# Kernel optimization log

Hardware: AMD Instinct MI355X
Metric: run time of the kernel (lower is better)

Reference implementation:

```python
import jax, jax.numpy as jnp
import numpy as np

NUM_CONCAT = 3

def setup_inputs() -> dict:
    key = jax.random.key(0)
    k1, k2, k3 = jax.random.split(key, 3)
    x = jax.random.normal(k1, (4, 2048, 4096), dtype=jnp.float32)
    W = jax.random.normal(k2, (12288, 4096), dtype=jnp.float32) * 0.02
    b = jax.random.normal(k3, (12288,), dtype=jnp.float32) * 0.02
    return {"x": x, "W": W, "b": b}

def reference(x, W, b):
    # Fused concat-linear: one GEMM over the concatenated weight, then split.
    # x: [B, S, D]; W: [NUM_CONCAT*H, D]; b: [NUM_CONCAT*H]
    y = jnp.einsum('bsd,od->bso', x, W) + b  # [B, S, NUM_CONCAT*H]
    hidden = y.shape[-1] // NUM_CONCAT
    return tuple(y[..., i * hidden:(i + 1) * hidden] for i in range(NUM_CONCAT))
```

## Files before the change

kernel.cpp:

```cpp
#include <hip/hip_runtime.h>
#include <stdint.h>


typedef __attribute__((ext_vector_type(8))) short short8;
typedef __attribute__((ext_vector_type(4))) float f32x4;

#define BM  256
#define BN  256
#define BKT 64

__device__ __forceinline__ unsigned short f2bf(float f) {
  union { float f; unsigned u; } v; v.f = f;
  unsigned u = v.u;
  u += 0x7FFFu + ((u >> 16) & 1u);
  return (unsigned short)(u >> 16);
}

__global__ __launch_bounds__(256)
void cast_all_f32_to_bf16(const float* __restrict__ a, unsigned long long na4,
                          unsigned short* __restrict__ oa,
                          const float* __restrict__ b, unsigned long long nb4,
                          unsigned short* __restrict__ ob) {
  const unsigned long long stride = (unsigned long long)gridDim.x * blockDim.x;
  const unsigned long long i0 = (unsigned long long)blockIdx.x * blockDim.x + threadIdx.x;
  for (unsigned long long k = i0; k < na4; k += stride) {
    float4 v = ((const float4*)a)[k];
    uint2 o;
    o.x = (unsigned)f2bf(v.x) | ((unsigned)f2bf(v.y) << 16);
    o.y = (unsigned)f2bf(v.z) | ((unsigned)f2bf(v.w) << 16);
    ((uint2*)oa)[k] = o;
  }
  for (unsigned long long k = i0; k < nb4; k += stride) {
    float4 v = ((const float4*)b)[k];
    uint2 o;
    o.x = (unsigned)f2bf(v.x) | ((unsigned)f2bf(v.y) << 16);
    o.y = (unsigned)f2bf(v.z) | ((unsigned)f2bf(v.w) << 16);
    ((uint2*)ob)[k] = o;
  }
}

__device__ __forceinline__ void gload16(const unsigned short* src, short* dst) {
  __builtin_amdgcn_global_load_lds(
      (const __attribute__((address_space(1))) unsigned int*)src,
      (__attribute__((address_space(3))) unsigned int*)dst, 16, 0, 0);
}

__global__ __launch_bounds__(512, 2)
void gemm256_bias_split(const unsigned short* __restrict__ A,
                        const unsigned short* __restrict__ B,
                        const float* __restrict__ bias,
                        float* __restrict__ out,
                        int M, int N, int K, int H) {
  __shared__ short smem[2 * BM * BKT + 2 * BN * BKT];
  short* const sA0 = smem;
  short* const sB0 = smem + 2 * BM * BKT;

  const int tid  = threadIdx.x;
  const int lane = tid & 63;
  const int r16  = lane & 15;
  const int q    = lane >> 4;
  const int wave = tid >> 6;
  const int wr   = wave >> 2;
  const int wc   = wave & 3;
  const int AR   = wr * 128;
  const int BR   = wc * 64;

  const int ntx = N / BN;
  const int nwg = gridDim.x;
  const int mty = nwg / ntx;
  int bid = blockIdx.x;
  int m0, n0;
  if ((nwg & 7) == 0 && (mty & 7) == 0) {
    const int GM  = mty >> 3;
    const int xcd = bid & 7;
    const int l   = bid >> 3;
    const int lm  = l % GM;
    const int ln  = l / GM;
    m0 = (xcd * GM + lm) * BM;
    n0 = ln * BN;
  } else if ((nwg & 7) == 0) {
    const int cpx = nwg >> 3;
    const int b2  = (bid & 7) * cpx + (bid >> 3);
    n0 = (b2 % ntx) * BN;
    m0 = (b2 / ntx) * BM;
  } else {
    n0 = (bid % ntx) * BN;
    m0 = (bid / ntx) * BM;
  }

  const int NT = K / BKT;

  const int c   = tid & 7;
  const int pr  = tid >> 3;
  const int csz = c ^ (pr & 7);
  const unsigned short* gA = A + (size_t)(m0 + pr) * K + csz * 8;
  const int prB = (pr & 31) + ((tid >> 8) << 6);
  const unsigned short* gB = B + (size_t)(n0 + prB) * K + csz * 8;
  const int dA = pr * 64 + c * 8;
  const int dB = prB * 64 + c * 8;
  const size_t K128 = (size_t)128 * K;

  auto stageA = [&](int buf, int kt, int u) {
    const unsigned short* s = gA + (size_t)(u * 64) * K + kt * BKT;
    short* d = sA0 + buf * (BM * BKT) + dA + u * 4096;
    gload16(s, d);
    gload16(s + K128, d + 8192);
  };
  auto stageB = [&](int buf, int kt, int u) {
    const unsigned short* s = gB + (size_t)(u * 32) * K + kt * BKT;
    short* d = sB0 + buf * (BN * BKT) + dB + u * 2048;
    gload16(s, d);
    gload16(s + K128, d + 8192);
  };

  const int swz  = r16 & 7;
  const int aoff = (AR + r16) * 64;
  const int boff = (BR + r16) * 64;
  const int ck0  = (q ^ swz) * 8;
  const int ck1  = ((4 + q) ^ swz) * 8;

  f32x4 acc[8][4];
#pragma unroll
  for (int i = 0; i < 8; ++i)
#pragma unroll
    for (int j = 0; j < 4; ++j) acc[i][j] = (f32x4){0.f, 0.f, 0.f, 0.f};

  stageA(0, 0, 0); stageB(0, 0, 0); stageA(0, 0, 1); stageB(0, 0, 1);
  stageA(1, 1, 0); stageB(1, 1, 0); stageA(1, 1, 1);
  asm volatile("s_waitcnt vmcnt(6)" ::: "memory");
  __builtin_amdgcn_s_barrier();

  short8 alo[4][2], ahi[4][2], b01[2][2], b23[2][2];

  for (int j = 0; j < NT; ++j) {
    const int P = j & 1;
    const short* bA = sA0 + P * (BM * BKT);
    const short* bB = sB0 + P * (BN * BKT);

#pragma unroll
    for (int mf = 0; mf < 4; ++mf) {
      alo[mf][0] = *(const short8*)&bA[aoff + mf * 1024 + ck0];
      alo[mf][1] = *(const short8*)&bA[aoff + mf * 1024 + ck1];
    }
#pragma unroll
    for (int nf = 0; nf < 2; ++nf) {
      b01[nf][0] = *(const short8*)&bB[boff + nf * 1024 + ck0];
      b01[nf][1] = *(const short8*)&bB[boff + nf * 1024 + ck1];
    }
    if (j + 1 < NT) stageB(P ^ 1, j + 1, 1);
    __builtin_amdgcn_s_barrier();
    asm volatile("s_waitcnt lgkmcnt(0)" ::: "memory");
    __builtin_amdgcn_sched_barrier(0);
    __builtin_amdgcn_s_setprio(1);
#pragma unroll
    for (int mf = 0; mf < 4; ++mf)
#pragma unroll
      for (int nf = 0; nf < 2; ++nf) {
        acc[mf][nf] = __builtin_amdgcn_mfma_f32_16x16x32_bf16(alo[mf][0], b01[nf][0], acc[mf][nf], 0, 0, 0);
        acc[mf][nf] = __builtin_amdgcn_mfma_f32_16x16x32_bf16(alo[mf][1], b01[nf][1], acc[mf][nf], 0, 0, 0);
      }
    __builtin_amdgcn_s_setprio(0);
    __builtin_amdgcn_s_barrier();

#pragma unroll
    for (int nf = 0; nf < 2; ++nf) {
      b23[nf][0] = *(const short8*)&bB[boff + (nf + 2) * 1024 + ck0];
      b23[nf][1] = *(const short8*)&bB[boff + (nf + 2) * 1024 + ck1];
    }
    if (j + 2 < NT) stageA(P, j + 2, 0);
    __builtin_amdgcn_s_barrier();
    asm volatile("s_waitcnt lgkmcnt(0)" ::: "memory");
    __builtin_amdgcn_sched_barrier(0);
    __builtin_amdgcn_s_setprio(1);
#pragma unroll
    for (int mf = 0; mf < 4; ++mf)
#pragma unroll
      for (int nf = 0; nf < 2; ++nf) {
        acc[mf][nf + 2] = __builtin_amdgcn_mfma_f32_16x16x32_bf16(alo[mf][0], b23[nf][0], acc[mf][nf + 2], 0, 0, 0);
        acc[mf][nf + 2] = __builtin_amdgcn_mfma_f32_16x16x32_bf16(alo[mf][1], b23[nf][1], acc[mf][nf + 2], 0, 0, 0);
      }
    __builtin_amdgcn_s_setprio(0);
    __builtin_amdgcn_s_barrier();

#pragma unroll
    for (int mf = 0; mf < 4; ++mf) {
      ahi[mf][0] = *(const short8*)&bA[aoff + (mf + 4) * 1024 + ck0];
      ahi[mf][1] = *(const short8*)&bA[aoff + (mf + 4) * 1024 + ck1];
    }
    if (j + 2 < NT) stageB(P, j + 2, 0);
    __builtin_amdgcn_s_barrier();
    asm volatile("s_waitcnt lgkmcnt(0)" ::: "memory");
    __builtin_amdgcn_sched_barrier(0);
    __builtin_amdgcn_s_setprio(1);
#pragma unroll
    for (int mf = 0; mf < 4; ++mf)
#pragma unroll
      for (int nf = 0; nf < 2; ++nf) {
        acc[mf + 4][nf + 2] = __builtin_amdgcn_mfma_f32_16x16x32_bf16(ahi[mf][0], b23[nf][0], acc[mf + 4][nf + 2], 0, 0, 0);
        acc[mf + 4][nf + 2] = __builtin_amdgcn_mfma_f32_16x16x32_bf16(ahi[mf][1], b23[nf][1], acc[mf + 4][nf + 2], 0, 0, 0);
      }
    __builtin_amdgcn_s_setprio(0);
    __builtin_amdgcn_s_barrier();

    if (j + 2 < NT) stageA(P, j + 2, 1);
    __builtin_amdgcn_s_barrier();
    __builtin_amdgcn_s_setprio(1);
#pragma unroll
    for (int mf = 0; mf < 4; ++mf)
#pragma unroll
      for (int nf = 0; nf < 2; ++nf) {
        acc[mf + 4][nf] = __builtin_amdgcn_mfma_f32_16x16x32_bf16(ahi[mf][0], b01[nf][0], acc[mf + 4][nf], 0, 0, 0);
        acc[mf + 4][nf] = __builtin_amdgcn_mfma_f32_16x16x32_bf16(ahi[mf][1], b01[nf][1], acc[mf + 4][nf], 0, 0, 0);
      }
    __builtin_amdgcn_s_setprio(0);
    if (j < NT - 2) asm volatile("s_waitcnt vmcnt(6)" ::: "memory");
    else            asm volatile("s_waitcnt vmcnt(0)" ::: "memory");
    __builtin_amdgcn_s_barrier();
  }

  float bj[4];
#pragma unroll
  for (int nf = 0; nf < 4; ++nf) bj[nf] = bias[n0 + BR + nf * 16 + r16];
  const int nb = n0 + BR;
  const int ci = nb / H;
  const int h0 = nb - ci * H;
  float* const obase = out + (size_t)ci * ((size_t)M * H) + h0;
  const int mbase = m0 + AR;
  float* const T = reinterpret_cast<float*>(smem) + wave * 4096;

#pragma unroll
  for (int p = 0; p < 2; ++p) {
#pragma unroll
    for (int mf = 0; mf < 4; ++mf)
#pragma unroll
      for (int nf = 0; nf < 4; ++nf)
#pragma unroll
        for (int rr = 0; rr < 4; ++rr)
          T[(mf * 16 + q * 4 + rr) * 64 + nf * 16 + r16] =
              acc[p * 4 + mf][nf][rr] + bj[nf];
    asm volatile("s_waitcnt lgkmcnt(0)" ::: "memory");
#pragma unroll
    for (int i = 0; i < 16; ++i) {
      const int row = i * 4 + q;
      float4 v = *(const float4*)&T[row * 64 + r16 * 4];
      *(float4*)&obase[(size_t)(mbase + p * 64 + row) * H + r16 * 4] = v;
    }
    asm volatile("s_waitcnt lgkmcnt(0)" ::: "memory");
  }
}

#define FTILE 128
#define FBK   64

__global__ __launch_bounds__(256)
void gemm_bias_split_fb(const float* __restrict__ Af32,
                        const float* __restrict__ Bf32,
                        const float* __restrict__ bias,
                        float* __restrict__ out,
                        int M, int N, int K, int H) {
  __shared__ short sA[FTILE * FBK];
  __shared__ short sB[FTILE * FBK];

  const int tid  = threadIdx.x;
  const int lane = tid & 63;
  const int r16  = lane & 15;
  const int q    = lane >> 4;
  const int wave = tid >> 6;
  const int wm   = (wave & 1) * 64;
  const int wn   = (wave >> 1) * 64;
  const int m0   = blockIdx.y * FTILE;
  const int n0   = blockIdx.x * FTILE;

  f32x4 acc[4][4];
#pragma unroll
  for (int i = 0; i < 4; ++i)
#pragma unroll
    for (int j = 0; j < 4; ++j)
      acc[i][j] = (f32x4){0.f, 0.f, 0.f, 0.f};

  for (int k0 = 0; k0 < K; k0 += FBK) {
    __syncthreads();
#pragma unroll
    for (int it = 0; it < 4; ++it) {
      const int chunk = it * 256 + tid;
      const int row   = chunk >> 3;
      const int c     = chunk & 7;
      const int cs    = c ^ (row & 7);
      const float* gA = Af32 + (size_t)(m0 + row) * K + (k0 + cs * 8);
      const float* gB = Bf32 + (size_t)(n0 + row) * K + (k0 + cs * 8);
      float4 a0 = ((const float4*)gA)[0], a1 = ((const float4*)gA)[1];
      float4 b0 = ((const float4*)gB)[0], b1 = ((const float4*)gB)[1];
      short8 va, vb;
      va[0] = (short)f2bf(a0.x); va[1] = (short)f2bf(a0.y);
      va[2] = (short)f2bf(a0.z); va[3] = (short)f2bf(a0.w);
      va[4] = (short)f2bf(a1.x); va[5] = (short)f2bf(a1.y);
      va[6] = (short)f2bf(a1.z); va[7] = (short)f2bf(a1.w);
      vb[0] = (short)f2bf(b0.x); vb[1] = (short)f2bf(b0.y);
      vb[2] = (short)f2bf(b0.z); vb[3] = (short)f2bf(b0.w);
      vb[4] = (short)f2bf(b1.x); vb[5] = (short)f2bf(b1.y);
      vb[6] = (short)f2bf(b1.z); vb[7] = (short)f2bf(b1.w);
      *(short8*)&sA[chunk * 8] = va;
      *(short8*)&sB[chunk * 8] = vb;
    }
    __syncthreads();

#pragma unroll
    for (int ks = 0; ks < 2; ++ks) {
      short8 af[4], bfr[4];
#pragma unroll
      for (int i = 0; i < 4; ++i) {
        const int row = wm + i * 16 + r16;
        const int cc  = ks * 4 + q;
        af[i] = *(const short8*)&sA[row * FBK + (cc ^ (row & 7)) * 8];
      }
#pragma unroll
      for (int j = 0; j < 4; ++j) {
        const int row = wn + j * 16 + r16;
        const int cc  = ks * 4 + q;
        bfr[j] = *(const short8*)&sB[row * FBK + (cc ^ (row & 7)) * 8];
      }
#pragma unroll
      for (int i = 0; i < 4; ++i)
#pragma unroll
        for (int j = 0; j < 4; ++j)
          acc[i][j] = __builtin_amdgcn_mfma_f32_16x16x32_bf16(
              af[i], bfr[j], acc[i][j], 0, 0, 0);
    }
  }

  float bj[4];
#pragma unroll
  for (int j = 0; j < 4; ++j) bj[j] = bias[n0 + wn + j * 16 + r16];
  const size_t chunk_elems = (size_t)M * H;
#pragma unroll
  for (int j = 0; j < 4; ++j) {
    const int n  = n0 + wn + j * 16 + r16;
    const int ci = n / H;
    const int h  = n - ci * H;
    float* obase = out + (size_t)ci * chunk_elems + h;
#pragma unroll
    for (int i = 0; i < 4; ++i) {
      const int mb = m0 + wm + i * 16 + q * 4;
#pragma unroll
      for (int rr = 0; rr < 4; ++rr) {
        obase[(size_t)(mb + rr) * H] = acc[i][j][rr] + bj[j];
      }
    }
  }
}

extern "C" void kernel_launch(void* const* d_in, const int* in_sizes, int n_in,
                              void* d_out, int out_size, void* d_ws, size_t ws_size,
                              hipStream_t stream) {
  const float* x = (const float*)d_in[0];
  const float* W = (const float*)d_in[1];
  const float* b = (const float*)d_in[2];
  float* out = (float*)d_out;

  const int N = in_sizes[2];
  const int K = in_sizes[1] / N;
  const int M = in_sizes[0] / K;
  const int H = N / 3;

  const size_t nA = (size_t)M * K;
  const size_t nB = (size_t)N * K;
  const bool ws_ok = ws_size >= (nA + nB) * sizeof(unsigned short);
  const bool big   = ws_ok && (M % BM == 0) && (N % BN == 0) &&
                     (K % BKT == 0) && (K / BKT >= 4) && ((H & 63) == 0);

  if (big) {
    unsigned short* xa = (unsigned short*)d_ws;
    unsigned short* wb = xa + nA;
    cast_all_f32_to_bf16<<<2048, 256, 0, stream>>>(
        x, (unsigned long long)(nA / 4), xa,
        W, (unsigned long long)(nB / 4), wb);
    const int nblocks = (M / BM) * (N / BN);
    gemm256_bias_split<<<nblocks, 512, 0, stream>>>(xa, wb, b, out, M, N, K, H);
  } else {
    dim3 grid(N / FTILE, M / FTILE);
    gemm_bias_split_fb<<<grid, 256, 0, stream>>>(x, W, b, out, M, N, K, H);
  }
}
```

Before: 1.245 ms.

## Software-pipeline LDS fragment reads one phase ahead of MFMA clusters

Register loads from shared memory are shifted one phase earlier: the B23 and A-high fragments are read before the preceding MFMA cluster, and the next tile's A-low and B01 fragments are prefetched at the end of the current iteration from the other buffer. Partial lgkmcnt waits replace full drains, so LDS latency is meant to overlap with matrix math. This moves a global vmcnt wait earlier and adds cross-iteration dependencies on buffer readiness, which risks races or extra stalls if the wait counts are wrong.

Measured after the change: 1.257 ms. About the same (+1.0%).

```diff
diff --git a/kernel.cpp b/kernel.cpp
--- a/kernel.cpp
+++ b/kernel.cpp
@@ -132,24 +132,34 @@
 
   short8 alo[4][2], ahi[4][2], b01[2][2], b23[2][2];
 
+#pragma unroll
+  for (int mf = 0; mf < 4; ++mf) {
+    alo[mf][0] = *(const short8*)&sA0[aoff + mf * 1024 + ck0];
+    alo[mf][1] = *(const short8*)&sA0[aoff + mf * 1024 + ck1];
+  }
+#pragma unroll
+  for (int nf = 0; nf < 2; ++nf) {
+    b01[nf][0] = *(const short8*)&sB0[boff + nf * 1024 + ck0];
+    b01[nf][1] = *(const short8*)&sB0[boff + nf * 1024 + ck1];
+  }
+  __builtin_amdgcn_sched_barrier(0);
+
   for (int j = 0; j < NT; ++j) {
     const int P = j & 1;
-    const short* bA = sA0 + P * (BM * BKT);
-    const short* bB = sB0 + P * (BN * BKT);
-
-#pragma unroll
-    for (int mf = 0; mf < 4; ++mf) {
-      alo[mf][0] = *(const short8*)&bA[aoff + mf * 1024 + ck0];
-      alo[mf][1] = *(const short8*)&bA[aoff + mf * 1024 + ck1];
-    }
+    const short* bA  = sA0 + P * (BM * BKT);
+    const short* bB  = sB0 + P * (BN * BKT);
+    const short* bA1 = sA0 + (P ^ 1) * (BM * BKT);
+    const short* bB1 = sB0 + (P ^ 1) * (BN * BKT);
+
+    if (j + 1 < NT) stageB(P ^ 1, j + 1, 1);
 #pragma unroll
     for (int nf = 0; nf < 2; ++nf) {
-      b01[nf][0] = *(const short8*)&bB[boff + nf * 1024 + ck0];
-      b01[nf][1] = *(const short8*)&bB[boff + nf * 1024 + ck1];
-    }
-    if (j + 1 < NT) stageB(P ^ 1, j + 1, 1);
-    __builtin_amdgcn_s_barrier();
-    asm volatile("s_waitcnt lgkmcnt(0)" ::: "memory");
+      b23[nf][0] = *(const short8*)&bB[boff + (nf + 2) * 1024 + ck0];
+      b23[nf][1] = *(const short8*)&bB[boff + (nf + 2) * 1024 + ck1];
+    }
+    __builtin_amdgcn_sched_barrier(0);
+    __builtin_amdgcn_s_barrier();
+    asm volatile("s_waitcnt lgkmcnt(4)" ::: "memory");
     __builtin_amdgcn_sched_barrier(0);
     __builtin_amdgcn_s_setprio(1);
 #pragma unroll
@@ -162,14 +172,15 @@
     __builtin_amdgcn_s_setprio(0);
     __builtin_amdgcn_s_barrier();
 
-#pragma unroll
-    for (int nf = 0; nf < 2; ++nf) {
-      b23[nf][0] = *(const short8*)&bB[boff + (nf + 2) * 1024 + ck0];
-      b23[nf][1] = *(const short8*)&bB[boff + (nf + 2) * 1024 + ck1];
-    }
     if (j + 2 < NT) stageA(P, j + 2, 0);
-    __builtin_amdgcn_s_barrier();
-    asm volatile("s_waitcnt lgkmcnt(0)" ::: "memory");
+#pragma unroll
+    for (int mf = 0; mf < 4; ++mf) {
+      ahi[mf][0] = *(const short8*)&bA[aoff + (mf + 4) * 1024 + ck0];
+      ahi[mf][1] = *(const short8*)&bA[aoff + (mf + 4) * 1024 + ck1];
+    }
+    __builtin_amdgcn_sched_barrier(0);
+    __builtin_amdgcn_s_barrier();
+    asm volatile("s_waitcnt lgkmcnt(8)" ::: "memory");
     __builtin_amdgcn_sched_barrier(0);
     __builtin_amdgcn_s_setprio(1);
 #pragma unroll
@@ -182,11 +193,6 @@
     __builtin_amdgcn_s_setprio(0);
     __builtin_amdgcn_s_barrier();
 
-#pragma unroll
-    for (int mf = 0; mf < 4; ++mf) {
-      ahi[mf][0] = *(const short8*)&bA[aoff + (mf + 4) * 1024 + ck0];
-      ahi[mf][1] = *(const short8*)&bA[aoff + (mf + 4) * 1024 + ck1];
-    }
     if (j + 2 < NT) stageB(P, j + 2, 0);
     __builtin_amdgcn_s_barrier();
     asm volatile("s_waitcnt lgkmcnt(0)" ::: "memory");
@@ -200,9 +206,19 @@
         acc[mf + 4][nf + 2] = __builtin_amdgcn_mfma_f32_16x16x32_bf16(ahi[mf][1], b23[nf][1], acc[mf + 4][nf + 2], 0, 0, 0);
       }
     __builtin_amdgcn_s_setprio(0);
+    if (j < NT - 2) asm volatile("s_waitcnt vmcnt(6)" ::: "memory");
+    else            asm volatile("s_waitcnt vmcnt(0)" ::: "memory");
     __builtin_amdgcn_s_barrier();
 
     if (j + 2 < NT) stageA(P, j + 2, 1);
+    if (j + 1 < NT) {
+#pragma unroll
+      for (int mf = 0; mf < 4; ++mf) {
+        alo[mf][0] = *(const short8*)&bA1[aoff + mf * 1024 + ck0];
+        alo[mf][1] = *(const short8*)&bA1[aoff + mf * 1024 + ck1];
+      }
+    }
+    __builtin_amdgcn_sched_barrier(0);
     __builtin_amdgcn_s_barrier();
     __builtin_amdgcn_s_setprio(1);
 #pragma unroll
@@ -213,6 +229,14 @@
         acc[mf + 4][nf] = __builtin_amdgcn_mfma_f32_16x16x32_bf16(ahi[mf][1], b01[nf][1], acc[mf + 4][nf], 0, 0, 0);
       }
     __builtin_amdgcn_s_setprio(0);
+    if (j + 1 < NT) {
+#pragma unroll
+      for (int nf = 0; nf < 2; ++nf) {
+        b01[nf][0] = *(const short8*)&bB1[boff + nf * 1024 + ck0];
+        b01[nf][1] = *(const short8*)&bB1[boff + nf * 1024 + ck1];
+      }
+    }
+    __builtin_amdgcn_sched_barrier(0);
     if (j < NT - 2) asm volatile("s_waitcnt vmcnt(6)" ::: "memory");
     else            asm volatile("s_waitcnt vmcnt(0)" ::: "memory");
     __builtin_amdgcn_s_barrier();
```
